# Performance work log

Hardware: AMD Instinct MI355X
Metric: run time of the kernel (lower is better)

Reference implementation:

```python
import math
import jax, jax.numpy as jnp
import numpy as np

DIM = 256
B = 32
M = 2048
N = 2048


def setup_inputs() -> dict:
    key = jax.random.key(0)
    k1, k2, k3, k4 = jax.random.split(key, 4)
    query = jax.random.normal(k1, (B, DIM, M), dtype=jnp.float32)
    key_t = jax.random.normal(k2, (B, DIM, N), dtype=jnp.float32)
    value = jax.random.normal(k3, (B, DIM, N), dtype=jnp.float32)
    # orthogonal random projection via QR, as in the torch __init__
    proj = np.asarray(jax.random.normal(k4, (DIM, DIM), dtype=jnp.float32))
    orth_proj, _ = np.linalg.qr(proj)
    orth_proj = jnp.asarray(orth_proj, dtype=jnp.float32)
    return {"query": query, "key": key_t, "value": value, "orth_proj": orth_proj}


def reference(query, key, value, orth_proj):
    dim = orth_proj.shape[0]
    q = query / math.sqrt(dim)
    # kernel feature maps: relu(W^T x), channels-first layout b c m
    phi_q = jax.nn.relu(jnp.einsum('bcm,ce->bem', q, orth_proj))
    phi_k = jax.nn.relu(jnp.einsum('bcn,ce->ben', key, orth_proj))
    phi_k_rowsum = phi_k.sum(-1)                         # [b, e]
    scale = jnp.einsum('bem,be->bm', phi_q, phi_k_rowsum)  # [b, m]
    scale = 1.0 / (scale + 1e-8)
    phi_q = phi_q * scale[:, None, :]                    # [b, e, m]
    kv = jnp.einsum('ben,bdn->bed', phi_k, value)        # [b, e, d]
    out = jnp.einsum('bem,bed->bdm', phi_q, kv)          # [b, d, m]
    return out
```

## Files before the change

kernel.cpp:

```cpp
#include <hip/hip_runtime.h>

#define DIMC 256
#define BSZ  32
#define MDIM 2048
#define NDIM 2048

typedef __attribute__((ext_vector_type(8))) short bf16x8;
typedef __attribute__((ext_vector_type(4))) float f32x4;

static __device__ __forceinline__ unsigned short f2bf(float x) {
  unsigned int u = __float_as_uint(x);
  u += 0x7fffu + ((u >> 16) & 1u);
  return (unsigned short)(u >> 16);
}
static __device__ __forceinline__ float bf2f(unsigned short h) {
  return __uint_as_float(((unsigned int)h) << 16);
}

__global__ __launch_bounds__(256) void wt_kernel(
    const float* __restrict__ W, unsigned short* __restrict__ Wt) {
  const int e = blockIdx.x, c = threadIdx.x;
  Wt[e * 256 + c] = f2bf(W[c * 256 + e]);
}

__global__ __launch_bounds__(256) void phik_kernel(
    const float* __restrict__ key, const unsigned short* __restrict__ Wt,
    unsigned short* __restrict__ phi_k) {
  __shared__ unsigned short As[128 * 40];
  __shared__ unsigned short Bs[128 * 40];
  const int b = blockIdx.z;
  const int n0 = blockIdx.x * 128;
  const int e0 = blockIdx.y * 128;
  const int t = threadIdx.x;
  const int lane = t & 63, wave = t >> 6;
  const int wr = wave >> 1, wc = wave & 1;
  const int q = lane >> 4, l15 = lane & 15;
  const float* keyb = key + (size_t)b * DIMC * NDIM;
  f32x4 acc[4][4];
#pragma unroll
  for (int i = 0; i < 4; ++i)
#pragma unroll
    for (int j = 0; j < 4; ++j) acc[i][j] = (f32x4){0.f, 0.f, 0.f, 0.f};

  const int arow = t >> 2, ac8 = (t & 3) << 3;
  const int nidx = t & 127, ch = (t >> 7) << 4;

  for (int k0 = 0; k0 < DIMC; k0 += 32) {
    __syncthreads();
    {
      uint4 v0 = *(const uint4*)(Wt + (size_t)(e0 + arow) * 256 + k0 + ac8);
      uint4 v1 = *(const uint4*)(Wt + (size_t)(e0 + arow + 64) * 256 + k0 + ac8);
      *(uint4*)&As[arow * 40 + ac8] = v0;
      *(uint4*)&As[(arow + 64) * 40 + ac8] = v1;
    }
    {
      const float* src = keyb + (size_t)(k0 + ch) * NDIM + n0 + nidx;
      unsigned short tmp[16] __attribute__((aligned(16)));
#pragma unroll
      for (int i = 0; i < 16; ++i) tmp[i] = f2bf(src[(size_t)i * NDIM]);
      *(uint4*)&Bs[nidx * 40 + ch] = *(const uint4*)&tmp[0];
      *(uint4*)&Bs[nidx * 40 + ch + 8] = *(const uint4*)&tmp[8];
    }
    __syncthreads();
    bf16x8 a[4], bv[4];
#pragma unroll
    for (int i = 0; i < 4; ++i)
      a[i] = *(const bf16x8*)&As[(wr * 64 + i * 16 + l15) * 40 + q * 8];
#pragma unroll
    for (int j = 0; j < 4; ++j)
      bv[j] = *(const bf16x8*)&Bs[(wc * 64 + j * 16 + l15) * 40 + q * 8];
#pragma unroll
    for (int i = 0; i < 4; ++i)
#pragma unroll
      for (int j = 0; j < 4; ++j)
        acc[i][j] =
            __builtin_amdgcn_mfma_f32_16x16x32_bf16(a[i], bv[j], acc[i][j], 0, 0, 0);
  }
  unsigned short* dst = phi_k + (size_t)b * DIMC * NDIM;
#pragma unroll
  for (int i = 0; i < 4; ++i)
#pragma unroll
    for (int j = 0; j < 4; ++j) {
      const int n = n0 + wc * 64 + j * 16 + l15;
#pragma unroll
      for (int r = 0; r < 4; ++r) {
        const int e = e0 + wr * 64 + i * 16 + q * 4 + r;
        float v = acc[i][j][r];
        dst[(size_t)e * NDIM + n] = f2bf(v > 0.f ? v : 0.f);
      }
    }
}

__global__ __launch_bounds__(256) void phiq_kernel(
    const float* __restrict__ query, const unsigned short* __restrict__ Wt,
    unsigned short* __restrict__ phi_q) {
  __shared__ unsigned short As[128 * 40];
  __shared__ unsigned short Bs[128 * 40];
  const int b = blockIdx.z;
  const int m0 = blockIdx.x * 128;
  const int e0 = blockIdx.y * 128;
  const int t = threadIdx.x;
  const int lane = t & 63, wave = t >> 6;
  const int wr = wave >> 1, wc = wave & 1;
  const int q = lane >> 4, l15 = lane & 15;
  const float* qb = query + (size_t)b * DIMC * MDIM;
  f32x4 acc[4][4];
#pragma unroll
  for (int i = 0; i < 4; ++i)
#pragma unroll
    for (int j = 0; j < 4; ++j) acc[i][j] = (f32x4){0.f, 0.f, 0.f, 0.f};

  const int brow = t >> 2, bc8 = (t & 3) << 3;
  const int midx = t & 127, ch = (t >> 7) << 4;

  for (int k0 = 0; k0 < DIMC; k0 += 32) {
    __syncthreads();
    {
      const float* src = qb + (size_t)(k0 + ch) * MDIM + m0 + midx;
      unsigned short tmp[16] __attribute__((aligned(16)));
#pragma unroll
      for (int i = 0; i < 16; ++i) tmp[i] = f2bf(src[(size_t)i * MDIM]);
      *(uint4*)&As[midx * 40 + ch] = *(const uint4*)&tmp[0];
      *(uint4*)&As[midx * 40 + ch + 8] = *(const uint4*)&tmp[8];
    }
    {
      uint4 v0 = *(const uint4*)(Wt + (size_t)(e0 + brow) * 256 + k0 + bc8);
      uint4 v1 = *(const uint4*)(Wt + (size_t)(e0 + brow + 64) * 256 + k0 + bc8);
      *(uint4*)&Bs[brow * 40 + bc8] = v0;
      *(uint4*)&Bs[(brow + 64) * 40 + bc8] = v1;
    }
    __syncthreads();
    bf16x8 a[4], bv[4];
#pragma unroll
    for (int i = 0; i < 4; ++i)
      a[i] = *(const bf16x8*)&As[(wr * 64 + i * 16 + l15) * 40 + q * 8];
#pragma unroll
    for (int j = 0; j < 4; ++j)
      bv[j] = *(const bf16x8*)&Bs[(wc * 64 + j * 16 + l15) * 40 + q * 8];
#pragma unroll
    for (int i = 0; i < 4; ++i)
#pragma unroll
      for (int j = 0; j < 4; ++j)
        acc[i][j] =
            __builtin_amdgcn_mfma_f32_16x16x32_bf16(a[i], bv[j], acc[i][j], 0, 0, 0);
  }
  unsigned short* dst = phi_q + (size_t)b * MDIM * DIMC;
#pragma unroll
  for (int i = 0; i < 4; ++i)
#pragma unroll
    for (int j = 0; j < 4; ++j) {
      const int e = e0 + wc * 64 + j * 16 + l15;
#pragma unroll
      for (int r = 0; r < 4; ++r) {
        const int m = m0 + wr * 64 + i * 16 + q * 4 + r;
        float v = acc[i][j][r];
        v = v > 0.f ? v * 0.0625f : 0.f;
        dst[(size_t)m * DIMC + e] = f2bf(v);
      }
    }
}

__global__ __launch_bounds__(256) void rowsum_kernel(
    const unsigned short* __restrict__ phi_k, float* __restrict__ rowsum) {
  const int row = blockIdx.x;
  const unsigned short* p = phi_k + (size_t)row * NDIM;
  uint4 v = *(const uint4*)(p + threadIdx.x * 8);
  const unsigned short* u = (const unsigned short*)&v;
  float s = 0.f;
#pragma unroll
  for (int i = 0; i < 8; ++i) s += bf2f(u[i]);
  __shared__ float red[256];
  red[threadIdx.x] = s;
  __syncthreads();
  for (int w = 128; w >= 1; w >>= 1) {
    if (threadIdx.x < w) red[threadIdx.x] += red[threadIdx.x + w];
    __syncthreads();
  }
  if (threadIdx.x == 0) rowsum[row] = red[0];
}

__global__ __launch_bounds__(256) void kv_kernel(
    const float* __restrict__ value, const unsigned short* __restrict__ phi_k,
    unsigned short* __restrict__ kv_t) {
  __shared__ unsigned short As[64 * 72];
  __shared__ unsigned short Bs[64 * 72];
  const int b = blockIdx.z;
  const int d0 = blockIdx.x * 64, e0 = blockIdx.y * 64;
  const int t = threadIdx.x;
  const int lane = t & 63, wave = t >> 6;
  const int wr = wave >> 1, wc = wave & 1;
  const int q = lane >> 4, l15 = lane & 15;
  f32x4 acc[2][2];
#pragma unroll
  for (int i = 0; i < 2; ++i)
#pragma unroll
    for (int j = 0; j < 2; ++j) acc[i][j] = (f32x4){0.f, 0.f, 0.f, 0.f};

  const int row = t >> 2, c16 = (t & 3) << 4;
  const float* asrc = value + ((size_t)b * DIMC + d0 + row) * NDIM + c16;
  const unsigned short* bsrc =
      phi_k + ((size_t)b * DIMC + e0 + row) * NDIM + c16;

  for (int n0 = 0; n0 < NDIM; n0 += 64) {
    __syncthreads();
    {
      float4 f0 = *(const float4*)(asrc + n0);
      float4 f1 = *(const float4*)(asrc + n0 + 4);
      float4 f2 = *(const float4*)(asrc + n0 + 8);
      float4 f3 = *(const float4*)(asrc + n0 + 12);
      unsigned short tmp[16] __attribute__((aligned(16)));
      tmp[0] = f2bf(f0.x); tmp[1] = f2bf(f0.y); tmp[2] = f2bf(f0.z); tmp[3] = f2bf(f0.w);
      tmp[4] = f2bf(f1.x); tmp[5] = f2bf(f1.y); tmp[6] = f2bf(f1.z); tmp[7] = f2bf(f1.w);
      tmp[8] = f2bf(f2.x); tmp[9] = f2bf(f2.y); tmp[10] = f2bf(f2.z); tmp[11] = f2bf(f2.w);
      tmp[12] = f2bf(f3.x); tmp[13] = f2bf(f3.y); tmp[14] = f2bf(f3.z); tmp[15] = f2bf(f3.w);
      *(uint4*)&As[row * 72 + c16] = *(const uint4*)&tmp[0];
      *(uint4*)&As[row * 72 + c16 + 8] = *(const uint4*)&tmp[8];
      uint4 b0 = *(const uint4*)(bsrc + n0);
      uint4 b1 = *(const uint4*)(bsrc + n0 + 8);
      *(uint4*)&Bs[row * 72 + c16] = b0;
      *(uint4*)&Bs[row * 72 + c16 + 8] = b1;
    }
    __syncthreads();
#pragma unroll
    for (int kk = 0; kk < 64; kk += 32) {
      bf16x8 a[2], bv[2];
#pragma unroll
      for (int i = 0; i < 2; ++i)
        a[i] = *(const bf16x8*)&As[(wr * 32 + i * 16 + l15) * 72 + kk + q * 8];
#pragma unroll
      for (int j = 0; j < 2; ++j)
        bv[j] = *(const bf16x8*)&Bs[(wc * 32 + j * 16 + l15) * 72 + kk + q * 8];
#pragma unroll
      for (int i = 0; i < 2; ++i)
#pragma unroll
        for (int j = 0; j < 2; ++j)
          acc[i][j] = __builtin_amdgcn_mfma_f32_16x16x32_bf16(a[i], bv[j],
                                                              acc[i][j], 0, 0, 0);
    }
  }
  unsigned short* dst = kv_t + (size_t)b * DIMC * DIMC;
#pragma unroll
  for (int i = 0; i < 2; ++i)
#pragma unroll
    for (int j = 0; j < 2; ++j) {
      const int e = e0 + wc * 32 + j * 16 + l15;
#pragma unroll
      for (int r = 0; r < 4; ++r) {
        const int d = d0 + wr * 32 + i * 16 + q * 4 + r;
        dst[(size_t)d * DIMC + e] = f2bf(acc[i][j][r]);
      }
    }
}

__global__ __launch_bounds__(256) void scale_kernel(
    const unsigned short* __restrict__ phi_q, const float* __restrict__ rowsum,
    float* __restrict__ scale) {
  const int gw = blockIdx.x * 4 + (threadIdx.x >> 6);
  const int b = gw >> 11, m = gw & 2047;
  const int lane = threadIdx.x & 63;
  const unsigned short* p = phi_q + ((size_t)b * MDIM + m) * DIMC + lane * 4;
  uint2 v = *(const uint2*)p;
  const unsigned short* u = (const unsigned short*)&v;
  float4 r = *(const float4*)(rowsum + b * DIMC + lane * 4);
  float s = bf2f(u[0]) * r.x + bf2f(u[1]) * r.y + bf2f(u[2]) * r.z +
            bf2f(u[3]) * r.w;
#pragma unroll
  for (int off = 32; off >= 1; off >>= 1) s += __shfl_down(s, off, 64);
  if (lane == 0) scale[(size_t)b * MDIM + m] = 1.f / (s + 1e-8f);
}

__global__ __launch_bounds__(256) void out_kernel(
    const unsigned short* __restrict__ kv_t,
    const unsigned short* __restrict__ phi_q, const float* __restrict__ scale,
    float* __restrict__ out) {
  __shared__ unsigned short As[128 * 40];
  __shared__ unsigned short Bs[128 * 40];
  const int b = blockIdx.z;
  const int m0 = blockIdx.x * 128;
  const int d0 = blockIdx.y * 128;
  const int t = threadIdx.x;
  const int lane = t & 63, wave = t >> 6;
  const int wr = wave >> 1, wc = wave & 1;
  const int q = lane >> 4, l15 = lane & 15;
  f32x4 acc[4][4];
#pragma unroll
  for (int i = 0; i < 4; ++i)
#pragma unroll
    for (int j = 0; j < 4; ++j) acc[i][j] = (f32x4){0.f, 0.f, 0.f, 0.f};

  const int row = t >> 2, c8 = (t & 3) << 3;
  const unsigned short* asrc = kv_t + ((size_t)b * DIMC + d0 + row) * DIMC + c8;
  const unsigned short* bsrc =
      phi_q + ((size_t)b * MDIM + m0 + row) * DIMC + c8;

  for (int k0 = 0; k0 < DIMC; k0 += 32) {
    __syncthreads();
    {
      uint4 a0 = *(const uint4*)(asrc + k0);
      uint4 a1 = *(const uint4*)(asrc + (size_t)64 * DIMC + k0);
      *(uint4*)&As[row * 40 + c8] = a0;
      *(uint4*)&As[(row + 64) * 40 + c8] = a1;
      uint4 b0 = *(const uint4*)(bsrc + k0);
      uint4 b1 = *(const uint4*)(bsrc + (size_t)64 * DIMC + k0);
      *(uint4*)&Bs[row * 40 + c8] = b0;
      *(uint4*)&Bs[(row + 64) * 40 + c8] = b1;
    }
    __syncthreads();
    bf16x8 a[4], bv[4];
#pragma unroll
    for (int i = 0; i < 4; ++i)
      a[i] = *(const bf16x8*)&As[(wr * 64 + i * 16 + l15) * 40 + q * 8];
#pragma unroll
    for (int j = 0; j < 4; ++j)
      bv[j] = *(const bf16x8*)&Bs[(wc * 64 + j * 16 + l15) * 40 + q * 8];
#pragma unroll
    for (int i = 0; i < 4; ++i)
#pragma unroll
      for (int j = 0; j < 4; ++j)
        acc[i][j] =
            __builtin_amdgcn_mfma_f32_16x16x32_bf16(a[i], bv[j], acc[i][j], 0, 0, 0);
  }
  float* ob = out + (size_t)b * DIMC * MDIM;
  const float* scb = scale + (size_t)b * MDIM;
#pragma unroll
  for (int j = 0; j < 4; ++j) {
    const int m = m0 + wc * 64 + j * 16 + l15;
    const float sc = scb[m];
#pragma unroll
    for (int i = 0; i < 4; ++i) {
#pragma unroll
      for (int r = 0; r < 4; ++r) {
        const int d = d0 + wr * 64 + i * 16 + q * 4 + r;
        ob[(size_t)d * MDIM + m] = acc[i][j][r] * sc;
      }
    }
  }
}

extern "C" void kernel_launch(void* const* d_in, const int* in_sizes, int n_in,
                              void* d_out, int out_size, void* d_ws, size_t ws_size,
                              hipStream_t stream) {
  const float* query = (const float*)d_in[0];
  const float* key   = (const float*)d_in[1];
  const float* value = (const float*)d_in[2];
  const float* W     = (const float*)d_in[3];
  float* out = (float*)d_out;

  unsigned short* Wt    = (unsigned short*)d_ws;
  unsigned short* phi_q = Wt + 65536;
  unsigned short* phi_k = phi_q + (size_t)BSZ * MDIM * DIMC;
  unsigned short* kv_t  = phi_k + (size_t)BSZ * DIMC * NDIM;
  float* rowsum = (float*)(kv_t + (size_t)BSZ * DIMC * DIMC);
  float* scale  = rowsum + BSZ * DIMC;

  hipLaunchKernelGGL(wt_kernel, dim3(256), dim3(256), 0, stream, W, Wt);
  hipLaunchKernelGGL(phiq_kernel, dim3(MDIM / 128, DIMC / 128, BSZ), dim3(256),
                     0, stream, query, Wt, phi_q);
  hipLaunchKernelGGL(phik_kernel, dim3(NDIM / 128, DIMC / 128, BSZ), dim3(256),
                     0, stream, key, Wt, phi_k);
  hipLaunchKernelGGL(rowsum_kernel, dim3(BSZ * DIMC), dim3(256), 0, stream,
                     phi_k, rowsum);
  hipLaunchKernelGGL(kv_kernel, dim3(DIMC / 64, DIMC / 64, BSZ), dim3(256), 0,
                     stream, value, phi_k, kv_t);
  hipLaunchKernelGGL(scale_kernel, dim3(BSZ * MDIM / 4), dim3(256), 0, stream,
                     phi_q, rowsum, scale);
  hipLaunchKernelGGL(out_kernel, dim3(MDIM / 128, DIMC / 128, BSZ), dim3(256),
                     0, stream, kv_t, phi_q, scale, out);
}
```

Baseline: 324.7 us.

## Use direct global-to-LDS loads, pre-convert value to bf16, split-K kv with atomics

```diff
diff --git a/kernel.cpp b/kernel.cpp
--- a/kernel.cpp
+++ b/kernel.cpp
@@ -17,16 +17,98 @@
   return __uint_as_float(((unsigned int)h) << 16);
 }
 
+static __device__ __forceinline__ void gl_lds16(const void* g, void* l) {
+  __builtin_amdgcn_global_load_lds(
+      (const __attribute__((address_space(1))) unsigned int*)g,
+      (__attribute__((address_space(3))) unsigned int*)l, 16, 0, 0);
+}
+
 __global__ __launch_bounds__(256) void wt_kernel(
     const float* __restrict__ W, unsigned short* __restrict__ Wt) {
   const int e = blockIdx.x, c = threadIdx.x;
   Wt[e * 256 + c] = f2bf(W[c * 256 + e]);
 }
 
+__global__ __launch_bounds__(256) void vconv_kernel(
+    const float* __restrict__ v, unsigned short* __restrict__ vb) {
+  const size_t i = ((size_t)blockIdx.x * 256 + threadIdx.x) * 8;
+  float4 a = *(const float4*)(v + i);
+  float4 b = *(const float4*)(v + i + 4);
+  unsigned short t[8] __attribute__((aligned(16)));
+  t[0] = f2bf(a.x); t[1] = f2bf(a.y); t[2] = f2bf(a.z); t[3] = f2bf(a.w);
+  t[4] = f2bf(b.x); t[5] = f2bf(b.y); t[6] = f2bf(b.z); t[7] = f2bf(b.w);
+  *(uint4*)(vb + i) = *(const uint4*)t;
+}
+
+__global__ __launch_bounds__(256) void phiq_kernel(
+    const float* __restrict__ X, const unsigned short* __restrict__ Wt,
+    unsigned short* __restrict__ phi) {
+  __shared__ unsigned short As[128 * 32];
+  __shared__ unsigned short Bs[128 * 40];
+  const int b = blockIdx.z;
+  const int m0 = blockIdx.x * 128;
+  const int e0 = blockIdx.y * 128;
+  const int t = threadIdx.x;
+  const int lane = t & 63, wave = t >> 6;
+  const int wr = wave >> 1, wc = wave & 1;
+  const int q = lane >> 4, l15 = lane & 15;
+  const float* Xb = X + (size_t)b * DIMC * MDIM;
+  const int a1row = t >> 2, a1k = (t & 3) << 3;
+  const int midx = t & 127, ch = (t >> 7) << 4;
+  f32x4 acc[4][4];
+#pragma unroll
+  for (int i = 0; i < 4; ++i)
+#pragma unroll
+    for (int j = 0; j < 4; ++j) acc[i][j] = (f32x4){0.f, 0.f, 0.f, 0.f};
+
+  for (int k0 = 0; k0 < DIMC; k0 += 32) {
+    __syncthreads();
+    gl_lds16(Wt + (size_t)(e0 + a1row) * DIMC + k0 + a1k, &As[wave * 512]);
+    gl_lds16(Wt + (size_t)(e0 + a1row + 64) * DIMC + k0 + a1k,
+             &As[2048 + wave * 512]);
+    {
+      const float* src = Xb + (size_t)(k0 + ch) * MDIM + m0 + midx;
+      unsigned short tmp[16] __attribute__((aligned(16)));
+#pragma unroll
+      for (int i = 0; i < 16; ++i) tmp[i] = f2bf(src[(size_t)i * MDIM]);
+      *(uint4*)&Bs[midx * 40 + ch] = *(const uint4*)&tmp[0];
+      *(uint4*)&Bs[midx * 40 + ch + 8] = *(const uint4*)&tmp[8];
+    }
+    __syncthreads();
+    bf16x8 a[4], bv[4];
+#pragma unroll
+    for (int i = 0; i < 4; ++i)
+      a[i] = *(const bf16x8*)&As[(wr * 64 + i * 16 + l15) * 32 + q * 8];
+#pragma unroll
+    for (int j = 0; j < 4; ++j)
+      bv[j] = *(const bf16x8*)&Bs[(wc * 64 + j * 16 + l15) * 40 + q * 8];
+#pragma unroll
+    for (int i = 0; i < 4; ++i)
+#pragma unroll
+      for (int j = 0; j < 4; ++j)
+        acc[i][j] =
+            __builtin_amdgcn_mfma_f32_16x16x32_bf16(a[i], bv[j], acc[i][j], 0, 0, 0);
+  }
+  unsigned short* dst = phi + (size_t)b * MDIM * DIMC;
+#pragma unroll
+  for (int i = 0; i < 4; ++i)
+#pragma unroll
+    for (int j = 0; j < 4; ++j) {
+      const int m = m0 + wc * 64 + j * 16 + l15;
+#pragma unroll
+      for (int r = 0; r < 4; ++r) {
+        const int e = e0 + wr * 64 + i * 16 + q * 4 + r;
+        float v = acc[i][j][r];
+        v = v > 0.f ? v * 0.0625f : 0.f;
+        dst[(size_t)m * DIMC + e] = f2bf(v);
+      }
+    }
+}
+
 __global__ __launch_bounds__(256) void phik_kernel(
-    const float* __restrict__ key, const unsigned short* __restrict__ Wt,
-    unsigned short* __restrict__ phi_k) {
-  __shared__ unsigned short As[128 * 40];
+    const float* __restrict__ X, const unsigned short* __restrict__ Wt,
+    unsigned short* __restrict__ phi) {
+  __shared__ unsigned short As[128 * 32];
   __shared__ unsigned short Bs[128 * 40];
   const int b = blockIdx.z;
   const int n0 = blockIdx.x * 128;
@@ -35,26 +117,22 @@
   const int lane = t & 63, wave = t >> 6;
   const int wr = wave >> 1, wc = wave & 1;
   const int q = lane >> 4, l15 = lane & 15;
-  const float* keyb = key + (size_t)b * DIMC * NDIM;
+  const float* Xb = X + (size_t)b * DIMC * NDIM;
+  const int a1row = t >> 2, a1k = (t & 3) << 3;
+  const int nidx = t & 127, ch = (t >> 7) << 4;
   f32x4 acc[4][4];
 #pragma unroll
   for (int i = 0; i < 4; ++i)
 #pragma unroll
     for (int j = 0; j < 4; ++j) acc[i][j] = (f32x4){0.f, 0.f, 0.f, 0.f};
 
-  const int arow = t >> 2, ac8 = (t & 3) << 3;
-  const int nidx = t & 127, ch = (t >> 7) << 4;
-
   for (int k0 = 0; k0 < DIMC; k0 += 32) {
     __syncthreads();
+    gl_lds16(Wt + (size_t)(e0 + a1row) * DIMC + k0 + a1k, &As[wave * 512]);
+    gl_lds16(Wt + (size_t)(e0 + a1row + 64) * DIMC + k0 + a1k,
+             &As[2048 + wave * 512]);
     {
-      uint4 v0 = *(const uint4*)(Wt + (size_t)(e0 + arow) * 256 + k0 + ac8);
-      uint4 v1 = *(const uint4*)(Wt + (size_t)(e0 + arow + 64) * 256 + k0 + ac8);
-      *(uint4*)&As[arow * 40 + ac8] = v0;
-      *(uint4*)&As[(arow + 64) * 40 + ac8] = v1;
-    }
-    {
-      const float* src = keyb + (size_t)(k0 + ch) * NDIM + n0 + nidx;
+      const float* src = Xb + (size_t)(k0 + ch) * NDIM + n0 + nidx;
       unsigned short tmp[16] __attribute__((aligned(16)));
 #pragma unroll
       for (int i = 0; i < 16; ++i) tmp[i] = f2bf(src[(size_t)i * NDIM]);
@@ -65,7 +143,7 @@
     bf16x8 a[4], bv[4];
 #pragma unroll
     for (int i = 0; i < 4; ++i)
-      a[i] = *(const bf16x8*)&As[(wr * 64 + i * 16 + l15) * 40 + q * 8];
+      a[i] = *(const bf16x8*)&As[(wr * 64 + i * 16 + l15) * 32 + q * 8];
 #pragma unroll
     for (int j = 0; j < 4; ++j)
       bv[j] = *(const bf16x8*)&Bs[(wc * 64 + j * 16 + l15) * 40 + q * 8];
@@ -76,7 +154,7 @@
         acc[i][j] =
             __builtin_amdgcn_mfma_f32_16x16x32_bf16(a[i], bv[j], acc[i][j], 0, 0, 0);
   }
-  unsigned short* dst = phi_k + (size_t)b * DIMC * NDIM;
+  unsigned short* dst = phi + (size_t)b * DIMC * NDIM;
 #pragma unroll
   for (int i = 0; i < 4; ++i)
 #pragma unroll
@@ -87,75 +165,6 @@
         const int e = e0 + wr * 64 + i * 16 + q * 4 + r;
         float v = acc[i][j][r];
         dst[(size_t)e * NDIM + n] = f2bf(v > 0.f ? v : 0.f);
-      }
-    }
-}
-
-__global__ __launch_bounds__(256) void phiq_kernel(
-    const float* __restrict__ query, const unsigned short* __restrict__ Wt,
-    unsigned short* __restrict__ phi_q) {
-  __shared__ unsigned short As[128 * 40];
-  __shared__ unsigned short Bs[128 * 40];
-  const int b = blockIdx.z;
-  const int m0 = blockIdx.x * 128;
-  const int e0 = blockIdx.y * 128;
-  const int t = threadIdx.x;
-  const int lane = t & 63, wave = t >> 6;
-  const int wr = wave >> 1, wc = wave & 1;
-  const int q = lane >> 4, l15 = lane & 15;
-  const float* qb = query + (size_t)b * DIMC * MDIM;
-  f32x4 acc[4][4];
-#pragma unroll
-  for (int i = 0; i < 4; ++i)
-#pragma unroll
-    for (int j = 0; j < 4; ++j) acc[i][j] = (f32x4){0.f, 0.f, 0.f, 0.f};
-
-  const int brow = t >> 2, bc8 = (t & 3) << 3;
-  const int midx = t & 127, ch = (t >> 7) << 4;
-
-  for (int k0 = 0; k0 < DIMC; k0 += 32) {
-    __syncthreads();
-    {
-      const float* src = qb + (size_t)(k0 + ch) * MDIM + m0 + midx;
-      unsigned short tmp[16] __attribute__((aligned(16)));
-#pragma unroll
-      for (int i = 0; i < 16; ++i) tmp[i] = f2bf(src[(size_t)i * MDIM]);
-      *(uint4*)&As[midx * 40 + ch] = *(const uint4*)&tmp[0];
-      *(uint4*)&As[midx * 40 + ch + 8] = *(const uint4*)&tmp[8];
-    }
-    {
-      uint4 v0 = *(const uint4*)(Wt + (size_t)(e0 + brow) * 256 + k0 + bc8);
-      uint4 v1 = *(const uint4*)(Wt + (size_t)(e0 + brow + 64) * 256 + k0 + bc8);
-      *(uint4*)&Bs[brow * 40 + bc8] = v0;
-      *(uint4*)&Bs[(brow + 64) * 40 + bc8] = v1;
-    }
-    __syncthreads();
-    bf16x8 a[4], bv[4];
-#pragma unroll
-    for (int i = 0; i < 4; ++i)
-      a[i] = *(const bf16x8*)&As[(wr * 64 + i * 16 + l15) * 40 + q * 8];
-#pragma unroll
-    for (int j = 0; j < 4; ++j)
-      bv[j] = *(const bf16x8*)&Bs[(wc * 64 + j * 16 + l15) * 40 + q * 8];
-#pragma unroll
-    for (int i = 0; i < 4; ++i)
-#pragma unroll
-      for (int j = 0; j < 4; ++j)
-        acc[i][j] =
-            __builtin_amdgcn_mfma_f32_16x16x32_bf16(a[i], bv[j], acc[i][j], 0, 0, 0);
-  }
-  unsigned short* dst = phi_q + (size_t)b * MDIM * DIMC;
-#pragma unroll
-  for (int i = 0; i < 4; ++i)
-#pragma unroll
-    for (int j = 0; j < 4; ++j) {
-      const int e = e0 + wc * 64 + j * 16 + l15;
-#pragma unroll
-      for (int r = 0; r < 4; ++r) {
-        const int m = m0 + wr * 64 + i * 16 + q * 4 + r;
-        float v = acc[i][j][r];
-        v = v > 0.f ? v * 0.0625f : 0.f;
-        dst[(size_t)m * DIMC + e] = f2bf(v);
       }
     }
 }
@@ -180,76 +189,71 @@
 }
 
 __global__ __launch_bounds__(256) void kv_kernel(
-    const float* __restrict__ value, const unsigned short* __restrict__ phi_k,
-    unsigned short* __restrict__ kv_t) {
-  __shared__ unsigned short As[64 * 72];
-  __shared__ unsigned short Bs[64 * 72];
-  const int b = blockIdx.z;
-  const int d0 = blockIdx.x * 64, e0 = blockIdx.y * 64;
+    const unsigned short* __restrict__ vb,
+    const unsigned short* __restrict__ phi_k, float* __restrict__ kv_acc) {
+  __shared__ unsigned short As[128 * 32];
+  __shared__ unsigned short Bs[128 * 32];
+  const int z = blockIdx.z;
+  const int b = z >> 2, slice = z & 3;
+  const int d0 = blockIdx.x * 128, e0 = blockIdx.y * 128;
   const int t = threadIdx.x;
   const int lane = t & 63, wave = t >> 6;
   const int wr = wave >> 1, wc = wave & 1;
   const int q = lane >> 4, l15 = lane & 15;
-  f32x4 acc[2][2];
-#pragma unroll
-  for (int i = 0; i < 2; ++i)
-#pragma unroll
-    for (int j = 0; j < 2; ++j) acc[i][j] = (f32x4){0.f, 0.f, 0.f, 0.f};
-
-  const int row = t >> 2, c16 = (t & 3) << 4;
-  const float* asrc = value + ((size_t)b * DIMC + d0 + row) * NDIM + c16;
-  const unsigned short* bsrc =
-      phi_k + ((size_t)b * DIMC + e0 + row) * NDIM + c16;
-
-  for (int n0 = 0; n0 < NDIM; n0 += 64) {
-    __syncthreads();
-    {
-      float4 f0 = *(const float4*)(asrc + n0);
-      float4 f1 = *(const float4*)(asrc + n0 + 4);
-      float4 f2 = *(const float4*)(asrc + n0 + 8);
-      float4 f3 = *(const float4*)(asrc + n0 + 12);
-      unsigned short tmp[16] __attribute__((aligned(16)));
-      tmp[0] = f2bf(f0.x); tmp[1] = f2bf(f0.y); tmp[2] = f2bf(f0.z); tmp[3] = f2bf(f0.w);
-      tmp[4] = f2bf(f1.x); tmp[5] = f2bf(f1.y); tmp[6] = f2bf(f1.z); tmp[7] = f2bf(f1.w);
-      tmp[8] = f2bf(f2.x); tmp[9] = f2bf(f2.y); tmp[10] = f2bf(f2.z); tmp[11] = f2bf(f2.w);
-      tmp[12] = f2bf(f3.x); tmp[13] = f2bf(f3.y); tmp[14] = f2bf(f3.z); tmp[15] = f2bf(f3.w);
-      *(uint4*)&As[row * 72 + c16] = *(const uint4*)&tmp[0];
-      *(uint4*)&As[row * 72 + c16 + 8] = *(const uint4*)&tmp[8];
-      uint4 b0 = *(const uint4*)(bsrc + n0);
-      uint4 b1 = *(const uint4*)(bsrc + n0 + 8);
-      *(uint4*)&Bs[row * 72 + c16] = b0;
-      *(uint4*)&Bs[row * 72 + c16 + 8] = b1;
-    }
-    __syncthreads();
-#pragma unroll
-    for (int kk = 0; kk < 64; kk += 32) {
-      bf16x8 a[2], bv[2];
-#pragma unroll
-      for (int i = 0; i < 2; ++i)
-        a[i] = *(const bf16x8*)&As[(wr * 32 + i * 16 + l15) * 72 + kk + q * 8];
-#pragma unroll
-      for (int j = 0; j < 2; ++j)
-        bv[j] = *(const bf16x8*)&Bs[(wc * 32 + j * 16 + l15) * 72 + kk + q * 8];
-#pragma unroll
-      for (int i = 0; i < 2; ++i)
-#pragma unroll
-        for (int j = 0; j < 2; ++j)
-          acc[i][j] = __builtin_amdgcn_mfma_f32_16x16x32_bf16(a[i], bv[j],
-                                                              acc[i][j], 0, 0, 0);
-    }
-  }
-  unsigned short* dst = kv_t + (size_t)b * DIMC * DIMC;
-#pragma unroll
-  for (int i = 0; i < 2; ++i)
-#pragma unroll
-    for (int j = 0; j < 2; ++j) {
-      const int e = e0 + wc * 32 + j * 16 + l15;
+  const unsigned short* Ab = vb + (size_t)b * DIMC * NDIM;
+  const unsigned short* Bb = phi_k + (size_t)b * DIMC * NDIM;
+  const int a1row = t >> 2, a1k = (t & 3) << 3;
+  f32x4 acc[4][4];
+#pragma unroll
+  for (int i = 0; i < 4; ++i)
+#pragma unroll
+    for (int j = 0; j < 4; ++j) acc[i][j] = (f32x4){0.f, 0.f, 0.f, 0.f};
+
+  const int nbeg = slice * 512;
+  for (int n0 = nbeg; n0 < nbeg + 512; n0 += 32) {
+    __syncthreads();
+    gl_lds16(Ab + (size_t)(d0 + a1row) * NDIM + n0 + a1k, &As[wave * 512]);
+    gl_lds16(Ab + (size_t)(d0 + a1row + 64) * NDIM + n0 + a1k,
+             &As[2048 + wave * 512]);
+    gl_lds16(Bb + (size_t)(e0 + a1row) * NDIM + n0 + a1k, &Bs[wave * 512]);
+    gl_lds16(Bb + (size_t)(e0 + a1row + 64) * NDIM + n0 + a1k,
+             &Bs[2048 + wave * 512]);
+    __syncthreads();
+    bf16x8 a[4], bv[4];
+#pragma unroll
+    for (int i = 0; i < 4; ++i)
+      a[i] = *(const bf16x8*)&As[(wr * 64 + i * 16 + l15) * 32 + q * 8];
+#pragma unroll
+    for (int j = 0; j < 4; ++j)
+      bv[j] = *(const bf16x8*)&Bs[(wc * 64 + j * 16 + l15) * 32 + q * 8];
+#pragma unroll
+    for (int i = 0; i < 4; ++i)
+#pragma unroll
+      for (int j = 0; j < 4; ++j)
+        acc[i][j] =
+            __builtin_amdgcn_mfma_f32_16x16x32_bf16(a[i], bv[j], acc[i][j], 0, 0, 0);
+  }
+  float* kva = kv_acc + (size_t)b * DIMC * DIMC;
+#pragma unroll
+  for (int i = 0; i < 4; ++i)
+#pragma unroll
+    for (int j = 0; j < 4; ++j) {
+      const int e = e0 + wc * 64 + j * 16 + l15;
 #pragma unroll
       for (int r = 0; r < 4; ++r) {
-        const int d = d0 + wr * 32 + i * 16 + q * 4 + r;
-        dst[(size_t)d * DIMC + e] = f2bf(acc[i][j][r]);
+        const int d = d0 + wr * 64 + i * 16 + q * 4 + r;
+        atomicAdd(&kva[(size_t)d * DIMC + e], acc[i][j][r]);
       }
     }
+}
+
+__global__ __launch_bounds__(256) void kvcvt_kernel(
+    const float* __restrict__ acc, unsigned short* __restrict__ kvt) {
+  const size_t i = ((size_t)blockIdx.x * 256 + threadIdx.x) * 4;
+  float4 a = *(const float4*)(acc + i);
+  unsigned short t[4] __attribute__((aligned(8)));
+  t[0] = f2bf(a.x); t[1] = f2bf(a.y); t[2] = f2bf(a.z); t[3] = f2bf(a.w);
+  *(uint2*)(kvt + i) = *(const uint2*)t;
 }
 
 __global__ __launch_bounds__(256) void scale_kernel(
@@ -273,8 +277,8 @@
     const unsigned short* __restrict__ kv_t,
     const unsigned short* __restrict__ phi_q, const float* __restrict__ scale,
     float* __restrict__ out) {
-  __shared__ unsigned short As[128 * 40];
-  __shared__ unsigned short Bs[128 * 40];
+  __shared__ unsigned short As[128 * 32];
+  __shared__ unsigned short Bs[128 * 32];
   const int b = blockIdx.z;
   const int m0 = blockIdx.x * 128;
   const int d0 = blockIdx.y * 128;
@@ -282,37 +286,31 @@
   const int lane = t & 63, wave = t >> 6;
   const int wr = wave >> 1, wc = wave & 1;
   const int q = lane >> 4, l15 = lane & 15;
+  const unsigned short* Ab = kv_t + (size_t)b * DIMC * DIMC;
+  const unsigned short* Bb = phi_q + (size_t)b * MDIM * DIMC;
+  const int a1row = t >> 2, a1k = (t & 3) << 3;
   f32x4 acc[4][4];
 #pragma unroll
   for (int i = 0; i < 4; ++i)
 #pragma unroll
     for (int j = 0; j < 4; ++j) acc[i][j] = (f32x4){0.f, 0.f, 0.f, 0.f};
 
-  const int row = t >> 2, c8 = (t & 3) << 3;
-  const unsigned short* asrc = kv_t + ((size_t)b * DIMC + d0 + row) * DIMC + c8;
-  const unsigned short* bsrc =
-      phi_q + ((size_t)b * MDIM + m0 + row) * DIMC + c8;
-
   for (int k0 = 0; k0 < DIMC; k0 += 32) {
     __syncthreads();
-    {
-      uint4 a0 = *(const uint4*)(asrc + k0);
-      uint4 a1 = *(const uint4*)(asrc + (size_t)64 * DIMC + k0);
-      *(uint4*)&As[row * 40 + c8] = a0;
-      *(uint4*)&As[(row + 64) * 40 + c8] = a1;
-      uint4 b0 = *(const uint4*)(bsrc + k0);
-      uint4 b1 = *(const uint4*)(bsrc + (size_t)64 * DIMC + k0);
-      *(uint4*)&Bs[row * 40 + c8] = b0;
-      *(uint4*)&Bs[(row + 64) * 40 + c8] = b1;
-    }
+    gl_lds16(Ab + (size_t)(d0 + a1row) * DIMC + k0 + a1k, &As[wave * 512]);
+    gl_lds16(Ab + (size_t)(d0 + a1row + 64) * DIMC + k0 + a1k,
+             &As[2048 + wave * 512]);
+    gl_lds16(Bb + (size_t)(m0 + a1row) * DIMC + k0 + a1k, &Bs[wave * 512]);
+    gl_lds16(Bb + (size_t)(m0 + a1row + 64) * DIMC + k0 + a1k,
+             &Bs[2048 + wave * 512]);
     __syncthreads();
     bf16x8 a[4], bv[4];
 #pragma unroll
     for (int i = 0; i < 4; ++i)
-      a[i] = *(const bf16x8*)&As[(wr * 64 + i * 16 + l15) * 40 + q * 8];
+      a[i] = *(const bf16x8*)&As[(wr * 64 + i * 16 + l15) * 32 + q * 8];
 #pragma unroll
     for (int j = 0; j < 4; ++j)
-      bv[j] = *(const bf16x8*)&Bs[(wc * 64 + j * 16 + l15) * 40 + q * 8];
+      bv[j] = *(const bf16x8*)&Bs[(wc * 64 + j * 16 + l15) * 32 + q * 8];
 #pragma unroll
     for (int i = 0; i < 4; ++i)
 #pragma unroll
@@ -347,21 +345,27 @@
   float* out = (float*)d_out;
 
   unsigned short* Wt    = (unsigned short*)d_ws;
-  unsigned short* phi_q = Wt + 65536;
+  unsigned short* v_bf  = Wt + 65536;
+  unsigned short* phi_q = v_bf + (size_t)BSZ * DIMC * NDIM;
   unsigned short* phi_k = phi_q + (size_t)BSZ * MDIM * DIMC;
   unsigned short* kv_t  = phi_k + (size_t)BSZ * DIMC * NDIM;
-  float* rowsum = (float*)(kv_t + (size_t)BSZ * DIMC * DIMC);
+  float* kv_acc = (float*)(kv_t + (size_t)BSZ * DIMC * DIMC);
+  float* rowsum = kv_acc + (size_t)BSZ * DIMC * DIMC;
   float* scale  = rowsum + BSZ * DIMC;
 
+  hipMemsetAsync(kv_acc, 0, (size_t)BSZ * DIMC * DIMC * sizeof(float), stream);
   hipLaunchKernelGGL(wt_kernel, dim3(256), dim3(256), 0, stream, W, Wt);
+  hipLaunchKernelGGL(vconv_kernel, dim3(8192), dim3(256), 0, stream, value, v_bf);
   hipLaunchKernelGGL(phiq_kernel, dim3(MDIM / 128, DIMC / 128, BSZ), dim3(256),
                      0, stream, query, Wt, phi_q);
   hipLaunchKernelGGL(phik_kernel, dim3(NDIM / 128, DIMC / 128, BSZ), dim3(256),
                      0, stream, key, Wt, phi_k);
   hipLaunchKernelGGL(rowsum_kernel, dim3(BSZ * DIMC), dim3(256), 0, stream,
                      phi_k, rowsum);
-  hipLaunchKernelGGL(kv_kernel, dim3(DIMC / 64, DIMC / 64, BSZ), dim3(256), 0,
-                     stream, value, phi_k, kv_t);
+  hipLaunchKernelGGL(kv_kernel, dim3(2, 2, BSZ * 4), dim3(256), 0, stream,
+                     v_bf, phi_k, kv_acc);
+  hipLaunchKernelGGL(kvcvt_kernel, dim3(2048), dim3(256), 0, stream, kv_acc,
+                     kv_t);
   hipLaunchKernelGGL(scale_kernel, dim3(BSZ * MDIM / 4), dim3(256), 0, stream,
                      phi_q, rowsum, scale);
   hipLaunchKernelGGL(out_kernel, dim3(MDIM / 128, DIMC / 128, BSZ), dim3(256),
```

Measured after the change: 332.7 us. 2.5% more time.
